# Kernel optimization log

Hardware: AMD Instinct MI355X
Metric: run time of the kernel (lower is better)

The kernel has to match this reference:

```python
import jax, jax.numpy as jnp
import numpy as np

ALPHA = 0.929
BETA = 15.99
TAU = 0.0
EPS = 1e-8


def setup_inputs() -> dict:
    key = jax.random.key(0)
    k1, k2 = jax.random.split(key)
    head_outputs = jax.random.normal(k1, (8, 2048, 16, 128), dtype=jnp.float32)
    G = jax.random.normal(k2, (16, 16), dtype=jnp.float32)
    return {"head_outputs": head_outputs, "G": G}


def reference(head_outputs, G):
    B, T, H, d_h = head_outputs.shape
    N = B * T
    outputs = head_outputs.reshape(N, H, d_h)
    mu = outputs.mean(axis=0, keepdims=True)
    # torch .std() is unbiased (ddof=1)
    sigma = outputs.std(axis=0, keepdims=True, ddof=1)
    O_tilde = (outputs - mu) / (sigma + EPS)  # (N, H, d_h)

    # All pairwise cross-correlations in one batched contraction: (H, H, d_h, d_h)
    C = jnp.einsum('nid,nje->ijde', O_tilde, O_tilde) / N
    diff = C - jnp.eye(d_h, dtype=C.dtype)  # subtract_identity=True
    pair_loss = jnp.sum(diff * diff, axis=(2, 3))  # (H, H)

    w = ALPHA + (1.0 - ALPHA) * jax.nn.softplus(-BETA * (G - TAU))  # (H, H)

    upper = jnp.triu(jnp.ones((H, H), dtype=C.dtype), k=1)  # i < j mask
    n_pairs = H * (H - 1) // 2
    loss = jnp.sum(upper * w * pair_loss) / n_pairs
    return loss
```

## Files before the change

### kernel.cpp

```cpp
#include <hip/hip_runtime.h>
#include <hip/hip_bf16.h>

#define N_TOK   16384
#define HDIM    2048
#define NH      16
#define DH      128
#define NPAIRS  120
#define KCHUNKS 8
#define NKT     (N_TOK / 64)
#define KT_PER_CHUNK (NKT / KCHUNKS)
#define KT128_PER_CHUNK (KT_PER_CHUNK / 2)
#define PANEL_BYTES 8192

#define SUM_OFF    0u
#define SUMSQ_OFF  8192u
#define PC_OFF     36864u
#define XT_OFF     7901184u

typedef float f32x4 __attribute__((ext_vector_type(4)));
typedef int   v8i   __attribute__((ext_vector_type(8)));
typedef int   v2i   __attribute__((ext_vector_type(2)));
typedef long long i64t;

#if __has_builtin(__builtin_amdgcn_cvt_pk_fp8_f32)
__device__ __forceinline__ unsigned pk4_fp8(float a, float b, float c, float d) {
    int w = __builtin_amdgcn_cvt_pk_fp8_f32(a, b, 0, false);
    w = __builtin_amdgcn_cvt_pk_fp8_f32(c, d, w, true);
    return (unsigned)w;
}
#else
__device__ __forceinline__ unsigned char f2e4m3_sw(float f) {
    unsigned u = __float_as_uint(f);
    unsigned s = (u >> 24) & 0x80u;
    unsigned a = u & 0x7fffffffu;
    if (a >= 0x43e00000u) return (unsigned char)(s | 0x7eu);
    if (a < 0x3c800000u) {
        float av = __uint_as_float(a);
        int q = (int)rintf(av * 512.0f);
        return (unsigned char)(s | (unsigned)q);
    }
    unsigned lsb = (a >> 20) & 1u;
    a += 0x7ffffu + lsb;
    int e8 = (int)(a >> 23) - 120;
    unsigned m = (a >> 20) & 7u;
    return (unsigned char)(s | ((unsigned)e8 << 3) | m);
}
__device__ __forceinline__ unsigned pk4_fp8(float a, float b, float c, float d) {
    return (unsigned)f2e4m3_sw(a) | ((unsigned)f2e4m3_sw(b) << 8) |
           ((unsigned)f2e4m3_sw(c) << 16) | ((unsigned)f2e4m3_sw(d) << 24);
}
#endif

__global__ __launch_bounds__(256)
void stats_transpose_kernel(const float* __restrict__ X,
                            float* __restrict__ sum, float* __restrict__ sumsq,
                            unsigned char* __restrict__ Xt) {
    __shared__ float tile[64][129];
    __shared__ float sred[4][32][8];
    const int h  = blockIdx.x;
    const int by = blockIdx.y;
    const int n0 = by * 64;
    const int tx = threadIdx.x;
    const int w  = tx >> 6, l = tx & 63;
    const int cq = tx & 31;
    const int rq0 = tx >> 5;

    float4 s  = make_float4(0.f, 0.f, 0.f, 0.f);
    float4 ss = make_float4(0.f, 0.f, 0.f, 0.f);
    #pragma unroll
    for (int it = 0; it < 8; ++it) {
        int r = it * 8 + rq0;
        float4 x = *(const float4*)(X + (size_t)(n0 + r) * HDIM + h * DH + cq * 4);
        s.x += x.x; s.y += x.y; s.z += x.z; s.w += x.w;
        ss.x += x.x * x.x; ss.y += x.y * x.y; ss.z += x.z * x.z; ss.w += x.w * x.w;
        tile[r][cq * 4 + 0] = x.x; tile[r][cq * 4 + 1] = x.y;
        tile[r][cq * 4 + 2] = x.z; tile[r][cq * 4 + 3] = x.w;
    }
    s.x += __shfl_down(s.x, 32);  s.y += __shfl_down(s.y, 32);
    s.z += __shfl_down(s.z, 32);  s.w += __shfl_down(s.w, 32);
    ss.x += __shfl_down(ss.x, 32); ss.y += __shfl_down(ss.y, 32);
    ss.z += __shfl_down(ss.z, 32); ss.w += __shfl_down(ss.w, 32);
    if (l < 32) {
        sred[w][l][0] = s.x;  sred[w][l][1] = s.y;
        sred[w][l][2] = s.z;  sred[w][l][3] = s.w;
        sred[w][l][4] = ss.x; sred[w][l][5] = ss.y;
        sred[w][l][6] = ss.z; sred[w][l][7] = ss.w;
    }
    __syncthreads();
    if (tx < 32) {
        float a0 = 0.f, a1 = 0.f, a2 = 0.f, a3 = 0.f;
        float b0 = 0.f, b1 = 0.f, b2 = 0.f, b3 = 0.f;
        #pragma unroll
        for (int w2 = 0; w2 < 4; ++w2) {
            a0 += sred[w2][tx][0]; a1 += sred[w2][tx][1];
            a2 += sred[w2][tx][2]; a3 += sred[w2][tx][3];
            b0 += sred[w2][tx][4]; b1 += sred[w2][tx][5];
            b2 += sred[w2][tx][6]; b3 += sred[w2][tx][7];
        }
        int c = h * DH + tx * 4;
        atomicAdd(&sum[c + 0], a0);  atomicAdd(&sum[c + 1], a1);
        atomicAdd(&sum[c + 2], a2);  atomicAdd(&sum[c + 3], a3);
        atomicAdd(&sumsq[c + 0], b0); atomicAdd(&sumsq[c + 1], b1);
        atomicAdd(&sumsq[c + 2], b2); atomicAdd(&sumsq[c + 3], b3);
    }
    unsigned char* panel = Xt + ((size_t)h * NKT + by) * PANEL_BYTES;
    #pragma unroll
    for (int it = 0; it < 2; ++it) {
        int q = it * 256 + tx;
        int c = q >> 2, o = q & 3;
        uint4 pk;
        pk.x = pk4_fp8(tile[o*16+ 0][c], tile[o*16+ 1][c], tile[o*16+ 2][c], tile[o*16+ 3][c]);
        pk.y = pk4_fp8(tile[o*16+ 4][c], tile[o*16+ 5][c], tile[o*16+ 6][c], tile[o*16+ 7][c]);
        pk.z = pk4_fp8(tile[o*16+ 8][c], tile[o*16+ 9][c], tile[o*16+10][c], tile[o*16+11][c]);
        pk.w = pk4_fp8(tile[o*16+12][c], tile[o*16+13][c], tile[o*16+14][c], tile[o*16+15][c]);
        uint4 outv = ((c >> 3) & 1) ? make_uint4(pk.z, pk.w, pk.x, pk.y) : pk;
        *(uint4*)(panel + c * 64 + o * 16) = outv;
    }
}

__device__ __forceinline__ void gload16(const void* gsrc, void* ldst) {
    __builtin_amdgcn_global_load_lds(
        (const __attribute__((address_space(1))) unsigned int*)gsrc,
        (__attribute__((address_space(3))) unsigned int*)ldst,
        16, 0, 0);
}

__device__ __forceinline__ v8i gather_frag(const unsigned char* rp,
                                           int o0, int o1, int o2, int o3) {
    v2i x0 = *(const v2i*)(rp + o0);
    v2i x1 = *(const v2i*)(rp + o1);
    v2i x2 = *(const v2i*)(rp + o2);
    v2i x3 = *(const v2i*)(rp + o3);
    v8i r;
    r[0] = x0[0]; r[1] = x0[1];
    r[2] = x1[0]; r[3] = x1[1];
    r[4] = x2[0]; r[5] = x2[1];
    r[6] = x3[0]; r[7] = x3[1];
    return r;
}

__global__ __launch_bounds__(256, 2)
void gram_kernel(const unsigned char* __restrict__ Xt, float* __restrict__ pairC) {
    const int kc = blockIdx.x;
    const int p  = blockIdx.y;
    int i = 0, rem = p;
    while (rem >= NH - 1 - i) { rem -= NH - 1 - i; ++i; }
    const int j = i + 1 + rem;

    __shared__ alignas(16) unsigned char lds[2 * 4 * PANEL_BYTES];

    const int tx = threadIdx.x;
    const int w  = tx >> 6, l = tx & 63;
    const int wm = w >> 1, wn = w & 1;
    const int l15 = l & 15, quad = l >> 4;

    unsigned int goff0, goff1;
    {
        int r0 = tx >> 2, cl0 = tx & 3;
        goff0 = (unsigned int)(r0 * 64 + (cl0 ^ ((r0 >> 1) & 3)) * 16);
        int cfl = 256 + tx;
        int r1 = cfl >> 2, cl1 = cfl & 3;
        goff1 = (unsigned int)(r1 * 64 + (cl1 ^ ((r1 >> 1) & 3)) * 16);
    }
    const int lo0 = w * 1024;
    const int lo1 = 4096 + w * 1024;
    const char* Abase = (const char*)Xt + ((size_t)i * NKT + (size_t)kc * KT_PER_CHUNK) * PANEL_BYTES;
    const char* Bbase = (const char*)Xt + ((size_t)j * NKT + (size_t)kc * KT_PER_CHUNK) * PANEL_BYTES;

    auto STAGE = [&](int kt2, char* base) {
        const char* pa = Abase + (size_t)(kt2 * 2) * PANEL_BYTES;
        const char* pb = Bbase + (size_t)(kt2 * 2) * PANEL_BYTES;
        gload16(pa + goff0,               base + lo0);
        gload16(pa + goff1,               base + lo1);
        gload16(pa + PANEL_BYTES + goff0, base + PANEL_BYTES + lo0);
        gload16(pa + PANEL_BYTES + goff1, base + PANEL_BYTES + lo1);
        gload16(pb + goff0,               base + 2 * PANEL_BYTES + lo0);
        gload16(pb + goff1,               base + 2 * PANEL_BYTES + lo1);
        gload16(pb + PANEL_BYTES + goff0, base + 3 * PANEL_BYTES + lo0);
        gload16(pb + PANEL_BYTES + goff1, base + 3 * PANEL_BYTES + lo1);
    };

    f32x4 acc[4][4];
    #pragma unroll
    for (int mi = 0; mi < 4; ++mi)
        #pragma unroll
        for (int ni = 0; ni < 4; ++ni)
            acc[mi][ni] = (f32x4){0.f, 0.f, 0.f, 0.f};

    const int usw = (l15 & 6) | (l15 >> 3);
    const int selP = quad >> 1;
    const int ub   = (quad & 1) * 4;
    const int puo0 = ((ub + 0) ^ usw) * 8;
    const int puo1 = ((ub + 1) ^ usw) * 8;
    const int puo2 = ((ub + 2) ^ usw) * 8;
    const int puo3 = ((ub + 3) ^ usw) * 8;
    const int rowA = (wm * 64 + l15) * 64;
    const int rowB = (wn * 64 + l15) * 64;
    const int offA = selP * PANEL_BYTES + rowA;
    const int offB = 2 * PANEL_BYTES + selP * PANEL_BYTES + rowB;

    STAGE(0, (char*)lds);
    asm volatile("s_waitcnt vmcnt(0)\n\ts_barrier" ::: "memory");

    int cur = 0;
    for (int kt = 0; kt < KT128_PER_CHUNK; ++kt) {
        if (kt + 1 < KT128_PER_CHUNK)
            STAGE(kt + 1, (char*)lds + (cur ^ 1) * (4 * PANEL_BYTES));

        const unsigned char* bufb = lds + cur * (4 * PANEL_BYTES);
        const unsigned char* laP = bufb + offA;
        const unsigned char* lbP = bufb + offB;

        v8i a0 = gather_frag(laP + 0 * 1024, puo0, puo1, puo2, puo3);
        v8i a1 = gather_frag(laP + 1 * 1024, puo0, puo1, puo2, puo3);
        v8i a2 = gather_frag(laP + 2 * 1024, puo0, puo1, puo2, puo3);
        v8i a3 = gather_frag(laP + 3 * 1024, puo0, puo1, puo2, puo3);
        #pragma unroll
        for (int ni = 0; ni < 4; ++ni) {
            v8i b = gather_frag(lbP + ni * 1024, puo0, puo1, puo2, puo3);
            acc[0][ni] = __builtin_amdgcn_mfma_scale_f32_16x16x128_f8f6f4(
                a0, b, acc[0][ni], 0, 0, 0, 0x7F7F7F7F, 0, 0x7F7F7F7F);
            acc[1][ni] = __builtin_amdgcn_mfma_scale_f32_16x16x128_f8f6f4(
                a1, b, acc[1][ni], 0, 0, 0, 0x7F7F7F7F, 0, 0x7F7F7F7F);
            acc[2][ni] = __builtin_amdgcn_mfma_scale_f32_16x16x128_f8f6f4(
                a2, b, acc[2][ni], 0, 0, 0, 0x7F7F7F7F, 0, 0x7F7F7F7F);
            acc[3][ni] = __builtin_amdgcn_mfma_scale_f32_16x16x128_f8f6f4(
                a3, b, acc[3][ni], 0, 0, 0, 0x7F7F7F7F, 0, 0x7F7F7F7F);
        }

        if (kt + 1 < KT128_PER_CHUNK)
            asm volatile("s_waitcnt vmcnt(0) lgkmcnt(0)\n\ts_barrier" ::: "memory");
        cur ^= 1;
    }

    float* pc = pairC + (size_t)p * (DH * DH);
    #pragma unroll
    for (int mi = 0; mi < 4; ++mi)
        #pragma unroll
        for (int ni = 0; ni < 4; ++ni)
            #pragma unroll
            for (int r = 0; r < 4; ++r) {
                int row = wm * 64 + mi * 16 + quad * 4 + r;
                int col = wn * 64 + ni * 16 + l15;
                atomicAdd(&pc[row * DH + col], acc[mi][ni][r]);
            }
}

__global__ void pair_reduce_kernel(const float* __restrict__ pairC, const float* __restrict__ G,
                                   const float* __restrict__ sum, const float* __restrict__ sumsq,
                                   float* __restrict__ out) {
    int p = blockIdx.x;
    int i = 0, rem = p;
    while (rem >= NH - 1 - i) { rem -= NH - 1 - i; ++i; }
    int j = i + 1 + rem;
    __shared__ float smui[DH], smuj[DH], sri[DH], srj[DH];
    {
        int t = threadIdx.x;
        int head = (t < DH) ? i : j;
        int d = t & (DH - 1);
        int c = head * DH + d;
        float m = sum[c] * (1.f / (float)N_TOK);
        float var = (sumsq[c] - (float)N_TOK * m * m) * (1.f / (float)(N_TOK - 1));
        var = fmaxf(var, 0.f);
        float r = 1.f / (sqrtf(var) + 1e-8f);
        if (t < DH) { smui[d] = m; sri[d] = r; }
        else        { smuj[d] = m; srj[d] = r; }
    }
    __syncthreads();
    const float invN = 1.f / (float)N_TOK;
    const float* pc = pairC + (size_t)p * (DH * DH);
    float s = 0.f;
    for (int idx = threadIdx.x; idx < DH * DH; idx += 256) {
        int d = idx >> 7, e = idx & 127;
        float cn = (pc[idx] * invN - smui[d] * smuj[e]) * sri[d] * srj[e];
        float diff = cn - ((d == e) ? 1.f : 0.f);
        s += diff * diff;
    }
    for (int o = 32; o; o >>= 1) s += __shfl_down(s, o);
    __shared__ float red[4];
    if ((threadIdx.x & 63) == 0) red[threadIdx.x >> 6] = s;
    __syncthreads();
    if (threadIdx.x == 0) {
        float t = red[0] + red[1] + red[2] + red[3];
        float x = -15.99f * (G[i * NH + j] - 0.0f);
        float sp = (x > 20.f) ? x : log1pf(expf(x));
        float wgt = 0.929f + (1.f - 0.929f) * sp;
        atomicAdd(out, wgt * t * (1.f / (float)NPAIRS));
    }
}

extern "C" void kernel_launch(void* const* d_in, const int* in_sizes, int n_in,
                              void* d_out, int out_size, void* d_ws, size_t ws_size,
                              hipStream_t stream) {
    const float* X = (const float*)d_in[0];
    const float* G = (const float*)d_in[1];
    float* out = (float*)d_out;
    char* ws = (char*)d_ws;

    float*         sum   = (float*)(ws + SUM_OFF);
    float*         sumsq = (float*)(ws + SUMSQ_OFF);
    float*         pairC = (float*)(ws + PC_OFF);
    unsigned char* Xt    = (unsigned char*)(ws + XT_OFF);

    hipMemsetAsync(ws + SUM_OFF, 0, 16384, stream);
    hipMemsetAsync(ws + PC_OFF, 0, (size_t)NPAIRS * DH * DH * 4, stream);
    hipMemsetAsync(d_out, 0, 4, stream);

    stats_transpose_kernel<<<dim3(16, 256), 256, 0, stream>>>(X, sum, sumsq, Xt);
    gram_kernel<<<dim3(KCHUNKS, NPAIRS), 256, 0, stream>>>(Xt, pairC);
    pair_reduce_kernel<<<NPAIRS, 256, 0, stream>>>(pairC, G, sum, sumsq, out);
}
```

Measured before the change: 288.3 us.

## Use 8-wave gram blocks and per-chunk partial slabs instead of atomics

The gram kernel moves from 4 to 8 waves per block, so each wave now computes a 64x32 tile instead of 64x64 and issues half as many staging loads. Instead of atomically adding into one shared per-pair buffer, each K-chunk writes its partial 128x128 result to its own slab. The reduce kernel sums the eight slabs with float4 loads. This removes the atomic contention and the memset of the accumulation buffer, at the cost of about 8x more workspace, extra HBM traffic in the reduce, and fewer MFMAs per fragment load in each wave.

```diff
diff --git a/kernel.cpp b/kernel.cpp
--- a/kernel.cpp
+++ b/kernel.cpp
@@ -15,7 +15,7 @@
 #define SUM_OFF    0u
 #define SUMSQ_OFF  8192u
 #define PC_OFF     36864u
-#define XT_OFF     7901184u
+#define XT_OFF     62951424u
 
 typedef float f32x4 __attribute__((ext_vector_type(4)));
 typedef int   v8i   __attribute__((ext_vector_type(8)));
@@ -139,8 +139,8 @@
     return r;
 }
 
-__global__ __launch_bounds__(256, 2)
-void gram_kernel(const unsigned char* __restrict__ Xt, float* __restrict__ pairC) {
+__global__ __launch_bounds__(512, 2)
+void gram_kernel(const unsigned char* __restrict__ Xt, float* __restrict__ pairP) {
     const int kc = blockIdx.x;
     const int p  = blockIdx.y;
     int i = 0, rem = p;
@@ -151,40 +151,32 @@
 
     const int tx = threadIdx.x;
     const int w  = tx >> 6, l = tx & 63;
-    const int wm = w >> 1, wn = w & 1;
+    const int wm = w >> 2, wn = w & 3;
     const int l15 = l & 15, quad = l >> 4;
 
-    unsigned int goff0, goff1;
+    unsigned int goff;
     {
         int r0 = tx >> 2, cl0 = tx & 3;
-        goff0 = (unsigned int)(r0 * 64 + (cl0 ^ ((r0 >> 1) & 3)) * 16);
-        int cfl = 256 + tx;
-        int r1 = cfl >> 2, cl1 = cfl & 3;
-        goff1 = (unsigned int)(r1 * 64 + (cl1 ^ ((r1 >> 1) & 3)) * 16);
-    }
-    const int lo0 = w * 1024;
-    const int lo1 = 4096 + w * 1024;
+        goff = (unsigned int)(r0 * 64 + (cl0 ^ ((r0 >> 1) & 3)) * 16);
+    }
+    const int lo = w * 1024;
     const char* Abase = (const char*)Xt + ((size_t)i * NKT + (size_t)kc * KT_PER_CHUNK) * PANEL_BYTES;
     const char* Bbase = (const char*)Xt + ((size_t)j * NKT + (size_t)kc * KT_PER_CHUNK) * PANEL_BYTES;
 
     auto STAGE = [&](int kt2, char* base) {
         const char* pa = Abase + (size_t)(kt2 * 2) * PANEL_BYTES;
         const char* pb = Bbase + (size_t)(kt2 * 2) * PANEL_BYTES;
-        gload16(pa + goff0,               base + lo0);
-        gload16(pa + goff1,               base + lo1);
-        gload16(pa + PANEL_BYTES + goff0, base + PANEL_BYTES + lo0);
-        gload16(pa + PANEL_BYTES + goff1, base + PANEL_BYTES + lo1);
-        gload16(pb + goff0,               base + 2 * PANEL_BYTES + lo0);
-        gload16(pb + goff1,               base + 2 * PANEL_BYTES + lo1);
-        gload16(pb + PANEL_BYTES + goff0, base + 3 * PANEL_BYTES + lo0);
-        gload16(pb + PANEL_BYTES + goff1, base + 3 * PANEL_BYTES + lo1);
+        gload16(pa + goff,               base + lo);
+        gload16(pa + PANEL_BYTES + goff, base + PANEL_BYTES + lo);
+        gload16(pb + goff,               base + 2 * PANEL_BYTES + lo);
+        gload16(pb + PANEL_BYTES + goff, base + 3 * PANEL_BYTES + lo);
     };
 
-    f32x4 acc[4][4];
+    f32x4 acc[4][2];
     #pragma unroll
     for (int mi = 0; mi < 4; ++mi)
         #pragma unroll
-        for (int ni = 0; ni < 4; ++ni)
+        for (int ni = 0; ni < 2; ++ni)
             acc[mi][ni] = (f32x4){0.f, 0.f, 0.f, 0.f};
 
     const int usw = (l15 & 6) | (l15 >> 3);
@@ -194,10 +186,8 @@
     const int puo1 = ((ub + 1) ^ usw) * 8;
     const int puo2 = ((ub + 2) ^ usw) * 8;
     const int puo3 = ((ub + 3) ^ usw) * 8;
-    const int rowA = (wm * 64 + l15) * 64;
-    const int rowB = (wn * 64 + l15) * 64;
-    const int offA = selP * PANEL_BYTES + rowA;
-    const int offB = 2 * PANEL_BYTES + selP * PANEL_BYTES + rowB;
+    const int offA = selP * PANEL_BYTES + (wm * 64 + l15) * 64;
+    const int offB = 2 * PANEL_BYTES + selP * PANEL_BYTES + (wn * 32 + l15) * 64;
 
     STAGE(0, (char*)lds);
     asm volatile("s_waitcnt vmcnt(0)\n\ts_barrier" ::: "memory");
@@ -216,7 +206,7 @@
         v8i a2 = gather_frag(laP + 2 * 1024, puo0, puo1, puo2, puo3);
         v8i a3 = gather_frag(laP + 3 * 1024, puo0, puo1, puo2, puo3);
         #pragma unroll
-        for (int ni = 0; ni < 4; ++ni) {
+        for (int ni = 0; ni < 2; ++ni) {
             v8i b = gather_frag(lbP + ni * 1024, puo0, puo1, puo2, puo3);
             acc[0][ni] = __builtin_amdgcn_mfma_scale_f32_16x16x128_f8f6f4(
                 a0, b, acc[0][ni], 0, 0, 0, 0x7F7F7F7F, 0, 0x7F7F7F7F);
@@ -233,20 +223,20 @@
         cur ^= 1;
     }
 
-    float* pc = pairC + (size_t)p * (DH * DH);
+    float* pc = pairP + ((size_t)kc * NPAIRS + (size_t)p) * (DH * DH);
     #pragma unroll
     for (int mi = 0; mi < 4; ++mi)
         #pragma unroll
-        for (int ni = 0; ni < 4; ++ni)
+        for (int ni = 0; ni < 2; ++ni)
             #pragma unroll
             for (int r = 0; r < 4; ++r) {
                 int row = wm * 64 + mi * 16 + quad * 4 + r;
-                int col = wn * 64 + ni * 16 + l15;
-                atomicAdd(&pc[row * DH + col], acc[mi][ni][r]);
+                int col = wn * 32 + ni * 16 + l15;
+                pc[row * DH + col] = acc[mi][ni][r];
             }
 }
 
-__global__ void pair_reduce_kernel(const float* __restrict__ pairC, const float* __restrict__ G,
+__global__ void pair_reduce_kernel(const float* __restrict__ pairP, const float* __restrict__ G,
                                    const float* __restrict__ sum, const float* __restrict__ sumsq,
                                    float* __restrict__ out) {
     int p = blockIdx.x;
@@ -268,13 +258,28 @@
     }
     __syncthreads();
     const float invN = 1.f / (float)N_TOK;
-    const float* pc = pairC + (size_t)p * (DH * DH);
+    const size_t SLAB = (size_t)NPAIRS * DH * DH;
+    const float* base = pairP + (size_t)p * (DH * DH);
     float s = 0.f;
-    for (int idx = threadIdx.x; idx < DH * DH; idx += 256) {
-        int d = idx >> 7, e = idx & 127;
-        float cn = (pc[idx] * invN - smui[d] * smuj[e]) * sri[d] * srj[e];
-        float diff = cn - ((d == e) ? 1.f : 0.f);
-        s += diff * diff;
+    for (int q = threadIdx.x; q < (DH * DH) / 4; q += 256) {
+        float4 v = ((const float4*)base)[q];
+        #pragma unroll
+        for (int kc = 1; kc < KCHUNKS; ++kc) {
+            float4 t = ((const float4*)(base + kc * SLAB))[q];
+            v.x += t.x; v.y += t.y; v.z += t.z; v.w += t.w;
+        }
+        int d = q >> 5;
+        int e0 = (q & 31) * 4;
+        float md = smui[d], rd = sri[d];
+        float cn, df;
+        cn = (v.x * invN - md * smuj[e0 + 0]) * rd * srj[e0 + 0];
+        df = cn - ((d == e0 + 0) ? 1.f : 0.f); s += df * df;
+        cn = (v.y * invN - md * smuj[e0 + 1]) * rd * srj[e0 + 1];
+        df = cn - ((d == e0 + 1) ? 1.f : 0.f); s += df * df;
+        cn = (v.z * invN - md * smuj[e0 + 2]) * rd * srj[e0 + 2];
+        df = cn - ((d == e0 + 2) ? 1.f : 0.f); s += df * df;
+        cn = (v.w * invN - md * smuj[e0 + 3]) * rd * srj[e0 + 3];
+        df = cn - ((d == e0 + 3) ? 1.f : 0.f); s += df * df;
     }
     for (int o = 32; o; o >>= 1) s += __shfl_down(s, o);
     __shared__ float red[4];
@@ -299,14 +304,13 @@
 
     float*         sum   = (float*)(ws + SUM_OFF);
     float*         sumsq = (float*)(ws + SUMSQ_OFF);
-    float*         pairC = (float*)(ws + PC_OFF);
+    float*         pairP = (float*)(ws + PC_OFF);
     unsigned char* Xt    = (unsigned char*)(ws + XT_OFF);
 
     hipMemsetAsync(ws + SUM_OFF, 0, 16384, stream);
-    hipMemsetAsync(ws + PC_OFF, 0, (size_t)NPAIRS * DH * DH * 4, stream);
     hipMemsetAsync(d_out, 0, 4, stream);
 
     stats_transpose_kernel<<<dim3(16, 256), 256, 0, stream>>>(X, sum, sumsq, Xt);
-    gram_kernel<<<dim3(KCHUNKS, NPAIRS), 256, 0, stream>>>(Xt, pairC);
-    pair_reduce_kernel<<<NPAIRS, 256, 0, stream>>>(pairC, G, sum, sumsq, out);
-}
+    gram_kernel<<<dim3(KCHUNKS, NPAIRS), 512, 0, stream>>>(Xt, pairP);
+    pair_reduce_kernel<<<NPAIRS, 256, 0, stream>>>(pairP, G, sum, sumsq, out);
+}
```

After: 245.9 us. -14.7%, faster.
